# Performance work log

Measured on AMD Instinct MI355X. Metric: run time of the kernel, lower is better.

Reference implementation:

```python
import jax, jax.numpy as jnp
import numpy as np
import math

B, T, C, H = 4, 2048, 1024, 16
D = C // H  # head dim = 64


def setup_inputs() -> dict:
    key = jax.random.key(0)
    k1, k2, k3, k4, k5 = jax.random.split(key, 5)
    scale = 1.0 / math.sqrt(C)
    return {
        "x": jax.random.normal(k1, (B, T, C), dtype=jnp.float32),
        "w_attn": jax.random.normal(k2, (C, 3 * C), dtype=jnp.float32) * scale,
        "b_attn": jax.random.normal(k3, (3 * C,), dtype=jnp.float32) * 0.02,
        "w_proj": jax.random.normal(k4, (C, C), dtype=jnp.float32) * scale,
        "b_proj": jax.random.normal(k5, (C,), dtype=jnp.float32) * 0.02,
    }


def reference(x, w_attn, b_attn, w_proj, b_proj):
    Bx, Tx, Cx = x.shape
    qkv = x @ w_attn + b_attn                      # [B,T,3C]
    q, k, v = jnp.split(qkv, 3, axis=-1)           # each [B,T,C]
    # reshape to [B,H,T,D]
    q = q.reshape(Bx, Tx, H, D).transpose(0, 2, 1, 3)
    k = k.reshape(Bx, Tx, H, D).transpose(0, 2, 1, 3)
    v = v.reshape(Bx, Tx, H, D).transpose(0, 2, 1, 3)
    att = jnp.einsum("bhqd,bhkd->bhqk", q, k) * (1.0 / math.sqrt(D))
    causal = jnp.tril(jnp.ones((Tx, Tx), dtype=bool))
    att = jnp.where(causal, att, -jnp.inf)
    att = jax.nn.softmax(att, axis=-1)
    y = jnp.einsum("bhqk,bhkd->bhqd", att, v)      # [B,H,T,D]
    y = y.transpose(0, 2, 1, 3).reshape(Bx, Tx, Cx)
    return y @ w_proj + b_proj
```

## Files before the change

kernel.cpp:

```cpp
#include <hip/hip_runtime.h>
#include <hip/hip_bf16.h>
#include <stdint.h>

typedef unsigned short u16;
typedef unsigned int u32;
typedef __attribute__((ext_vector_type(8))) __bf16 bf16x8;
typedef __attribute__((ext_vector_type(4))) float f32x4;
typedef __attribute__((ext_vector_type(16))) float f32x16;

#define B_ 4
#define T_ 2048
#define C_ 1024
#define H_ 16
#define D_ 64

__device__ __forceinline__ u16 f2bf(float f) {
  union { float f; u32 u; } v; v.f = f;
  u32 r = (v.u + 0x7fffu + ((v.u >> 16) & 1u)) >> 16;
  return (u16)r;
}

__device__ __forceinline__ float fexp2(float x) {
  float r;
  asm("v_exp_f32 %0, %1\n\ts_nop 0" : "=v"(r) : "v"(x));
  return r;
}

__device__ __forceinline__ u32 cvtpk(float lo, float hi2) {
  u32 r;
  asm("v_cvt_pk_bf16_f32 %0, %1, %2" : "=v"(r) : "v"(lo), "v"(hi2));
  return r;
}

__device__ __forceinline__ void gll16(const void* g, void* l) {
  __builtin_amdgcn_global_load_lds((const __attribute__((address_space(1))) void*)g,
                                   (__attribute__((address_space(3))) void*)l, 16, 0, 0);
}

__global__ void k_prep(const float* __restrict__ x, u16* __restrict__ xb,
                       const float* __restrict__ wa, u16* __restrict__ waT,
                       const float* __restrict__ wp, u16* __restrict__ wpT) {
  __shared__ float tile[32][33];
  const int bid = blockIdx.x;
  const int tx = threadIdx.x, ty = threadIdx.y;
  if (bid < 2048) {
    const int tid = bid * 256 + ty * 32 + tx;
    const int n4 = (B_ * T_ * C_) / 4;
    for (int i = tid; i < n4; i += 2048 * 256) {
      float4 v = ((const float4*)x)[i];
      ushort4 o;
      o.x = f2bf(v.x); o.y = f2bf(v.y); o.z = f2bf(v.z); o.w = f2bf(v.w);
      ((ushort4*)xb)[i] = o;
    }
    return;
  }
  const float* src; u16* dst; int N, b2;
  if (bid < 5120) { b2 = bid - 2048; src = wa; dst = waT; N = 3 * C_; }
  else            { b2 = bid - 5120; src = wp; dst = wpT; N = C_; }
  const int K = C_;
  const int k0 = (b2 & 31) * 32, n0 = (b2 >> 5) * 32;
#pragma unroll
  for (int r = 0; r < 4; ++r) {
    int k = ty + r * 8;
    tile[k][tx] = src[(size_t)(k0 + k) * N + n0 + tx];
  }
  __syncthreads();
#pragma unroll
  for (int r = 0; r < 4; ++r) {
    int n = ty + r * 8;
    dst[(size_t)(n0 + n) * K + k0 + tx] = f2bf(tile[tx][n]);
  }
}

template <int MODE>
__global__ __launch_bounds__(256) void k_gemm(
    const u16* __restrict__ A, const u16* __restrict__ BT, const float* __restrict__ bias,
    float* __restrict__ outF, u16* __restrict__ qb, u16* __restrict__ kb, u16* __restrict__ vbT,
    int M, int N, int K) {
  __shared__ u16 al[3][128 * 32];
  __shared__ u16 bl[3][128 * 32];
  const int lane = threadIdx.x & 63, wid = threadIdx.x >> 6;
  const int nbx = N >> 7;
  const int cpx = ((M >> 7) * nbx) >> 3;
  const int wg = blockIdx.x;
  const int lid = (wg & 7) * cpx + (wg >> 3);
  const int brow = (lid / nbx) * 128, bcol = (lid % nbx) * 128;
  const int wr = (wid >> 1) * 64, wc = (wid & 1) * 64;
  const int lr = lane & 15, lg = lane >> 4;
  const int ck = (lg ^ ((lr >> 1) & 3)) * 8;
  f32x4 acc[4][4] = {};

  auto stage = [&](u16* ad, u16* bd, int t2) {
    const int kt = t2 * 32;
#pragma unroll
    for (int it = 0; it < 2; ++it) {
      int cbase = (wid * 2 + it) * 64;
      int c = cbase + lane;
      int row = c >> 2;
      int j = (c & 3) ^ ((row >> 1) & 3);
      int col = j * 8;
      gll16(A + (size_t)(brow + row) * K + kt + col, ad + cbase * 8);
      gll16(BT + (size_t)(bcol + row) * K + kt + col, bd + cbase * 8);
    }
  };

  const int nt = K / 32;
  stage(al[0], bl[0], 0);
  stage(al[1], bl[1], 1);

  for (int t = 0; t < nt; ++t) {
    if (t == nt - 1) { asm volatile("s_waitcnt vmcnt(0)" ::: "memory"); }
    else             { asm volatile("s_waitcnt vmcnt(4)" ::: "memory"); }
    __builtin_amdgcn_sched_barrier(0);
    __builtin_amdgcn_s_barrier();
    __builtin_amdgcn_sched_barrier(0);

    const int nxt = t + 2;
    if (nxt < nt) {
      const int ib = nxt % 3;
      stage(al[ib], bl[ib], nxt);
    }

    const u16* ab = al[t % 3];
    const u16* bb = bl[t % 3];
    bf16x8 af[4], bfr[4];
#pragma unroll
    for (int m = 0; m < 4; ++m) af[m] = *(const bf16x8*)&ab[(wr + m * 16 + lr) * 32 + ck];
#pragma unroll
    for (int n = 0; n < 4; ++n) bfr[n] = *(const bf16x8*)&bb[(wc + n * 16 + lr) * 32 + ck];

    __builtin_amdgcn_s_setprio(1);
#pragma unroll
    for (int m = 0; m < 4; ++m)
#pragma unroll
      for (int n = 0; n < 4; ++n)
        acc[m][n] = __builtin_amdgcn_mfma_f32_16x16x32_bf16(af[m], bfr[n], acc[m][n], 0, 0, 0);
    __builtin_amdgcn_s_setprio(0);
  }

#pragma unroll
  for (int m = 0; m < 4; ++m) {
    int row = brow + wr + m * 16 + lg * 4;
#pragma unroll
    for (int n = 0; n < 4; ++n) {
      int col = bcol + wc + n * 16 + lr;
      float bs = bias[col];
      if (MODE == 0) {
#pragma unroll
        for (int r = 0; r < 4; ++r)
          outF[(size_t)(row + r) * N + col] = acc[m][n][r] + bs;
      } else {
        int sec = col >> 10, cc = col & 1023;
        int h = cc >> 6, dd = cc & 63;
        int b = row >> 11, t = row & 2047;
        size_t bh = (size_t)(b * H_ + h);
        if (sec < 2) {
          u16* dst = (sec == 0 ? qb : kb) + (bh * T_ + t) * D_ + dd;
#pragma unroll
          for (int r = 0; r < 4; ++r) dst[(size_t)r * D_] = f2bf(acc[m][n][r] + bs);
        } else {
          ushort4 pk;
          pk.x = f2bf(acc[m][n][0] + bs);
          pk.y = f2bf(acc[m][n][1] + bs);
          pk.z = f2bf(acc[m][n][2] + bs);
          pk.w = f2bf(acc[m][n][3] + bs);
          *(ushort4*)&vbT[(bh * D_ + dd) * T_ + t] = pk;
        }
      }
    }
  }
}

__global__ __launch_bounds__(256) void k_attn(
    const u16* __restrict__ qb, const u16* __restrict__ kb,
    const u16* __restrict__ vbT, u16* __restrict__ attb) {
  __shared__ u16 kl0[64 * 64], kl1[64 * 64];
  __shared__ u16 vl0[64 * 64], vl1[64 * 64];
  const int lane = threadIdx.x & 63, wid = threadIdx.x >> 6;
  const int w = blockIdx.x;
  const int lid = (w & 7) * 64 + (w >> 3);
  const int bh = lid >> 3, qpair = lid & 7;
  const int b = bh >> 4, h = bh & 15;
  const int l31 = lane & 31, hi = lane >> 5;
  const int sw3 = l31 & 7;

  const float SC = 0.18033688f;

  const u16* kbase = kb + (size_t)bh * T_ * D_;
  const u16* vbase = vbT + (size_t)bh * D_ * T_;

  auto stage = [&](u16* kd, u16* vd, int kt) {
    const int k0 = kt * 64;
#pragma unroll
    for (int it = 0; it < 2; ++it) {
      int cbase = (wid * 2 + it) * 64;
      int c = cbase + lane;
      int cs = (c & ~7) | ((c ^ (c >> 3)) & 7);
      gll16(kbase + (size_t)k0 * D_ + (size_t)cs * 8, kd + cbase * 8);
      int vrow = cs >> 3, vcol = (cs & 7) * 8;
      gll16(vbase + (size_t)vrow * T_ + k0 + vcol, vd + cbase * 8);
    }
  };

  auto pack = [&](const f32x16& s, bf16x8* out) {
#pragma unroll
    for (int cc = 0; cc < 2; ++cc) {
      const int rb = cc * 8;
      u32 a  = cvtpk(s[rb + 0], s[rb + 1]);
      u32 c  = cvtpk(s[rb + 2], s[rb + 3]);
      u32 bb = cvtpk(s[rb + 4], s[rb + 5]);
      u32 d  = cvtpk(s[rb + 6], s[rb + 7]);
      u32 as = __shfl_xor(a, 32, 64), cs = __shfl_xor(c, 32, 64);
      u32 bs = __shfl_xor(bb, 32, 64), ds = __shfl_xor(d, 32, 64);
      union { u32 u[4]; bf16x8 v; } t;
      t.u[0] = hi ? bs : a;
      t.u[1] = hi ? ds : c;
      t.u[2] = hi ? bb : as;
      t.u[3] = hi ? d : cs;
      out[cc] = t.v;
    }
  };

#pragma unroll 1
  for (int pass = 0; pass < 2; ++pass) {
    const int qbk = pass ? (15 - qpair) : qpair;
    const int qw = qbk * 128 + wid * 32;

    const u16* qrow = qb + ((size_t)bh * T_ + qw + l31) * D_ + hi * 8;
    bf16x8 qf[4];
#pragma unroll
    for (int j = 0; j < 4; ++j) qf[j] = *(const bf16x8*)(qrow + j * 16);

    float lsum = 0.f;
    f32x16 o0 = {}, o1 = {};

    const int nt = 2 * qbk + 2;
    const int lastkt = (qw + 31) >> 6;

    auto compute = [&](const u16* kl, const u16* vl, int kt) {
      const int k0 = kt * 64;
      f32x16 s0 = {}, s1 = {};
      __builtin_amdgcn_s_setprio(1);
#pragma unroll
      for (int j = 0; j < 4; ++j) {
        const int ch = ((2 * j + hi) ^ sw3) << 3;
        const bf16x8 kf0 = *(const bf16x8*)&kl[l31 * 64 + ch];
        const bf16x8 kf1 = *(const bf16x8*)&kl[(l31 + 32) * 64 + ch];
        s0 = __builtin_amdgcn_mfma_f32_32x32x16_bf16(kf0, qf[j], s0, 0, 0, 0);
        s1 = __builtin_amdgcn_mfma_f32_32x32x16_bf16(kf1, qf[j], s1, 0, 0, 0);
      }
      __builtin_amdgcn_s_setprio(0);

      if (kt == lastkt) {
        const int q = qw + l31;
#pragma unroll
        for (int r = 0; r < 16; ++r) {
          const int kv = k0 + (r & 3) + 8 * (r >> 2) + 4 * hi;
          if (kv > q) s0[r] = -3e38f;
          if (kv + 32 > q) s1[r] = -3e38f;
        }
      }

#pragma unroll
      for (int r = 0; r < 16; ++r) s0[r] = fexp2(s0[r] * SC);
      float t0[8];
#pragma unroll
      for (int r = 0; r < 8; ++r) t0[r] = s0[r] + s0[r + 8];
#pragma unroll
      for (int w2 = 4; w2 >= 1; w2 >>= 1)
#pragma unroll
        for (int r = 0; r < 4; ++r)
          if (r < w2) t0[r] += t0[r + w2];

      bf16x8 pb0[2];
      pack(s0, pb0);
      __builtin_amdgcn_s_setprio(1);
#pragma unroll
      for (int c = 0; c < 2; ++c) {
        const int ch = ((2 * c + hi) ^ sw3) << 3;
        const bf16x8 vf0 = *(const bf16x8*)&vl[l31 * 64 + ch];
        const bf16x8 vf1 = *(const bf16x8*)&vl[(l31 + 32) * 64 + ch];
        o0 = __builtin_amdgcn_mfma_f32_32x32x16_bf16(vf0, pb0[c], o0, 0, 0, 0);
        o1 = __builtin_amdgcn_mfma_f32_32x32x16_bf16(vf1, pb0[c], o1, 0, 0, 0);
      }
      __builtin_amdgcn_s_setprio(0);

#pragma unroll
      for (int r = 0; r < 16; ++r) s1[r] = fexp2(s1[r] * SC);
      float t1[8];
#pragma unroll
      for (int r = 0; r < 8; ++r) t1[r] = s1[r] + s1[r + 8];
#pragma unroll
      for (int w2 = 4; w2 >= 1; w2 >>= 1)
#pragma unroll
        for (int r = 0; r < 4; ++r)
          if (r < w2) t1[r] += t1[r + w2];

      bf16x8 pb1[2];
      pack(s1, pb1);
      __builtin_amdgcn_s_setprio(1);
#pragma unroll
      for (int c = 2; c < 4; ++c) {
        const int ch = ((2 * c + hi) ^ sw3) << 3;
        const bf16x8 vf0 = *(const bf16x8*)&vl[l31 * 64 + ch];
        const bf16x8 vf1 = *(const bf16x8*)&vl[(l31 + 32) * 64 + ch];
        o0 = __builtin_amdgcn_mfma_f32_32x32x16_bf16(vf0, pb1[c - 2], o0, 0, 0, 0);
        o1 = __builtin_amdgcn_mfma_f32_32x32x16_bf16(vf1, pb1[c - 2], o1, 0, 0, 0);
      }
      __builtin_amdgcn_s_setprio(0);

      float ps = t0[0] + t1[0];
      ps += __shfl_xor(ps, 32, 64);
      lsum += ps;
    };

    stage(kl0, vl0, 0);
    __syncthreads();
    int kt = 0;
    while (true) {
      if (kt + 1 < nt) stage(kl1, vl1, kt + 1);
      if (kt <= lastkt) compute(kl0, vl0, kt);
      __syncthreads();
      if (++kt >= nt) break;
      if (kt + 1 < nt) stage(kl0, vl0, kt + 1);
      if (kt <= lastkt) compute(kl1, vl1, kt);
      __syncthreads();
      if (++kt >= nt) break;
    }

    const float inv = 1.0f / lsum;
    u16* orow = attb + ((size_t)b * T_ + qw + l31) * C_ + h * D_;
#pragma unroll
    for (int rg = 0; rg < 4; ++rg) {
      ushort4 w0, w1;
      w0.x = f2bf(o0[rg * 4 + 0] * inv); w0.y = f2bf(o0[rg * 4 + 1] * inv);
      w0.z = f2bf(o0[rg * 4 + 2] * inv); w0.w = f2bf(o0[rg * 4 + 3] * inv);
      w1.x = f2bf(o1[rg * 4 + 0] * inv); w1.y = f2bf(o1[rg * 4 + 1] * inv);
      w1.z = f2bf(o1[rg * 4 + 2] * inv); w1.w = f2bf(o1[rg * 4 + 3] * inv);
      const int d0 = rg * 8 + hi * 4;
      *(ushort4*)(orow + d0) = w0;
      *(ushort4*)(orow + d0 + 32) = w1;
    }
  }
}

extern "C" void kernel_launch(void* const* d_in, const int* in_sizes, int n_in,
                              void* d_out, int out_size, void* d_ws, size_t ws_size,
                              hipStream_t stream) {
  const float* x = (const float*)d_in[0];
  const float* w_attn = (const float*)d_in[1];
  const float* b_attn = (const float*)d_in[2];
  const float* w_proj = (const float*)d_in[3];
  const float* b_proj = (const float*)d_in[4];
  float* out = (float*)d_out;

  char* ws = (char*)d_ws;
  const size_t MB = 1024 * 1024;
  u16* xb   = (u16*)(ws);
  u16* attb = xb;
  u16* waT  = (u16*)(ws + 16 * MB);
  u16* wpT  = (u16*)(ws + 22 * MB);
  u16* qb   = (u16*)(ws + 24 * MB);
  u16* kb   = (u16*)(ws + 40 * MB);
  u16* vbT  = (u16*)(ws + 56 * MB);

  k_prep<<<6144, dim3(32, 8), 0, stream>>>(x, xb, w_attn, waT, w_proj, wpT);

  k_gemm<1><<<(8192 / 128) * (3 * C_ / 128), 256, 0, stream>>>(
      xb, waT, b_attn, nullptr, qb, kb, vbT, B_ * T_, 3 * C_, C_);

  k_attn<<<512, 256, 0, stream>>>(qb, kb, vbT, attb);

  k_gemm<0><<<(8192 / 128) * (C_ / 128), 256, 0, stream>>>(
      attb, wpT, b_proj, out, nullptr, nullptr, nullptr, B_ * T_, C_, C_);
}
```

Baseline: 167.5 us.

## Use 256x128 block tile GEMM for the QKV projection

Adds a new GEMM kernel with a 256x128 output tile per workgroup, where each wave computes 128x64 (8x4 MFMA tiles). It keeps a triple-buffered LDS pipeline with swizzled direct global-to-LDS loads, and uses it for the QKV projection. The larger tile raises arithmetic intensity per staged K-slice and halves the number of workgroups. In exchange it uses more accumulator registers and LDS per block, which may lower occupancy.

```diff
diff --git a/kernel.cpp b/kernel.cpp
--- a/kernel.cpp
+++ b/kernel.cpp
@@ -69,6 +69,110 @@
   for (int r = 0; r < 4; ++r) {
     int n = ty + r * 8;
     dst[(size_t)(n0 + n) * K + k0 + tx] = f2bf(tile[tx][n]);
+  }
+}
+
+template <int MODE>
+__global__ __launch_bounds__(256, 2) void k_gemmw(
+    const u16* __restrict__ A, const u16* __restrict__ BT, const float* __restrict__ bias,
+    float* __restrict__ outF, u16* __restrict__ qb, u16* __restrict__ kb, u16* __restrict__ vbT,
+    int M, int N, int K) {
+  __shared__ u16 al[3][256 * 32];
+  __shared__ u16 bl[3][128 * 32];
+  const int tid = threadIdx.x;
+  const int lane = tid & 63, wid = tid >> 6;
+  const int wm = wid >> 1, wn = wid & 1;
+  const int nbx = N >> 7;
+  const int cpx = ((M >> 8) * nbx) >> 3;
+  const int wg = blockIdx.x;
+  const int lid = (wg & 7) * cpx + (wg >> 3);
+  const int brow = (lid / nbx) * 256, bcol = (lid % nbx) * 128;
+  const int lr = lane & 15, lg = lane >> 4;
+  const int ck = (lg ^ ((lr >> 1) & 3)) * 8;
+  f32x4 acc[8][4] = {};
+
+  auto stage = [&](u16* ad, u16* bd, int t2) {
+    const int kt = t2 * 32;
+#pragma unroll
+    for (int it = 0; it < 4; ++it) {
+      int s = it * 256 + tid;
+      int row = s >> 2;
+      int j = (s & 3) ^ ((row >> 1) & 3);
+      gll16(A + (size_t)(brow + row) * K + kt + j * 8, ad + (s & ~63) * 8);
+    }
+#pragma unroll
+    for (int it = 0; it < 2; ++it) {
+      int s = it * 256 + tid;
+      int row = s >> 2;
+      int j = (s & 3) ^ ((row >> 1) & 3);
+      gll16(BT + (size_t)(bcol + row) * K + kt + j * 8, bd + (s & ~63) * 8);
+    }
+  };
+
+  const int nt = K / 32;
+  stage(al[0], bl[0], 0);
+  stage(al[1], bl[1], 1);
+
+  for (int t = 0; t < nt; ++t) {
+    if (t == nt - 1) { asm volatile("s_waitcnt vmcnt(0)" ::: "memory"); }
+    else             { asm volatile("s_waitcnt vmcnt(6)" ::: "memory"); }
+    __builtin_amdgcn_sched_barrier(0);
+    __builtin_amdgcn_s_barrier();
+    __builtin_amdgcn_sched_barrier(0);
+
+    const int nxt = t + 2;
+    if (nxt < nt) {
+      const int ib = nxt % 3;
+      stage(al[ib], bl[ib], nxt);
+    }
+
+    const u16* ab = al[t % 3];
+    const u16* bb = bl[t % 3];
+    bf16x8 af[8], bfr[4];
+#pragma unroll
+    for (int m = 0; m < 8; ++m) af[m] = *(const bf16x8*)&ab[(wm * 128 + m * 16 + lr) * 32 + ck];
+#pragma unroll
+    for (int n = 0; n < 4; ++n) bfr[n] = *(const bf16x8*)&bb[(wn * 64 + n * 16 + lr) * 32 + ck];
+
+    __builtin_amdgcn_s_setprio(1);
+#pragma unroll
+    for (int m = 0; m < 8; ++m)
+#pragma unroll
+      for (int n = 0; n < 4; ++n)
+        acc[m][n] = __builtin_amdgcn_mfma_f32_16x16x32_bf16(af[m], bfr[n], acc[m][n], 0, 0, 0);
+    __builtin_amdgcn_s_setprio(0);
+  }
+
+#pragma unroll
+  for (int m = 0; m < 8; ++m) {
+    int row = brow + wm * 128 + m * 16 + lg * 4;
+#pragma unroll
+    for (int n = 0; n < 4; ++n) {
+      int col = bcol + wn * 64 + n * 16 + lr;
+      float bs = bias[col];
+      if (MODE == 0) {
+#pragma unroll
+        for (int r = 0; r < 4; ++r)
+          outF[(size_t)(row + r) * N + col] = acc[m][n][r] + bs;
+      } else {
+        int sec = col >> 10, cc = col & 1023;
+        int h = cc >> 6, dd = cc & 63;
+        int b = row >> 11, t = row & 2047;
+        size_t bh = (size_t)(b * H_ + h);
+        if (sec < 2) {
+          u16* dst = (sec == 0 ? qb : kb) + (bh * T_ + t) * D_ + dd;
+#pragma unroll
+          for (int r = 0; r < 4; ++r) dst[(size_t)r * D_] = f2bf(acc[m][n][r] + bs);
+        } else {
+          ushort4 pk;
+          pk.x = f2bf(acc[m][n][0] + bs);
+          pk.y = f2bf(acc[m][n][1] + bs);
+          pk.z = f2bf(acc[m][n][2] + bs);
+          pk.w = f2bf(acc[m][n][3] + bs);
+          *(ushort4*)&vbT[(bh * D_ + dd) * T_ + t] = pk;
+        }
+      }
+    }
   }
 }
 
@@ -366,7 +470,7 @@
 
   k_prep<<<6144, dim3(32, 8), 0, stream>>>(x, xb, w_attn, waT, w_proj, wpT);
 
-  k_gemm<1><<<(8192 / 128) * (3 * C_ / 128), 256, 0, stream>>>(
+  k_gemmw<1><<<(8192 / 256) * (3 * C_ / 128), 256, 0, stream>>>(
       xb, waT, b_attn, nullptr, qb, kb, vbT, B_ * T_, 3 * C_, C_);
 
   k_attn<<<512, 256, 0, stream>>>(qb, kb, vbT, attb);
```

Result: slower. 180.7 us (+7.9%).

## Load K/V fragments directly from global memory instead of LDS double-buffering

Applied to the files above, without the earlier changes.

Removes the shared-memory double-buffered staging of K and V tiles and the block-wide barriers. Each wave now reads its MFMA operand fragments straight from global memory and stops at its own last causal tile instead of the block's. This drops LDS traffic and __syncthreads, but each of the four waves re-fetches the same K/V data through the cache, and the loads are no longer prefetched asynchronously ahead of compute. Global-load latency now sits directly in the MFMA dependency chain.

```diff
diff --git a/kernel.cpp b/kernel.cpp
--- a/kernel.cpp
+++ b/kernel.cpp
@@ -174,33 +174,21 @@
 __global__ __launch_bounds__(256) void k_attn(
     const u16* __restrict__ qb, const u16* __restrict__ kb,
     const u16* __restrict__ vbT, u16* __restrict__ attb) {
-  __shared__ u16 kl0[64 * 64], kl1[64 * 64];
-  __shared__ u16 vl0[64 * 64], vl1[64 * 64];
   const int lane = threadIdx.x & 63, wid = threadIdx.x >> 6;
   const int w = blockIdx.x;
   const int lid = (w & 7) * 64 + (w >> 3);
   const int bh = lid >> 3, qpair = lid & 7;
   const int b = bh >> 4, h = bh & 15;
   const int l31 = lane & 31, hi = lane >> 5;
-  const int sw3 = l31 & 7;
 
   const float SC = 0.18033688f;
 
   const u16* kbase = kb + (size_t)bh * T_ * D_;
   const u16* vbase = vbT + (size_t)bh * D_ * T_;
-
-  auto stage = [&](u16* kd, u16* vd, int kt) {
-    const int k0 = kt * 64;
-#pragma unroll
-    for (int it = 0; it < 2; ++it) {
-      int cbase = (wid * 2 + it) * 64;
-      int c = cbase + lane;
-      int cs = (c & ~7) | ((c ^ (c >> 3)) & 7);
-      gll16(kbase + (size_t)k0 * D_ + (size_t)cs * 8, kd + cbase * 8);
-      int vrow = cs >> 3, vcol = (cs & 7) * 8;
-      gll16(vbase + (size_t)vrow * T_ + k0 + vcol, vd + cbase * 8);
-    }
-  };
+  const u16* kr0 = kbase + (size_t)l31 * D_ + hi * 8;
+  const u16* kr1 = kbase + (size_t)(l31 + 32) * D_ + hi * 8;
+  const u16* vr0 = vbase + (size_t)l31 * T_ + hi * 8;
+  const u16* vr1 = vbase + (size_t)(l31 + 32) * T_ + hi * 8;
 
   auto pack = [&](const f32x16& s, bf16x8* out) {
 #pragma unroll
@@ -234,18 +222,19 @@
     float lsum = 0.f;
     f32x16 o0 = {}, o1 = {};
 
-    const int nt = 2 * qbk + 2;
     const int lastkt = (qw + 31) >> 6;
 
-    auto compute = [&](const u16* kl, const u16* vl, int kt) {
+#pragma unroll 1
+    for (int kt = 0; kt <= lastkt; ++kt) {
       const int k0 = kt * 64;
       f32x16 s0 = {}, s1 = {};
+      const u16* ka = kr0 + (size_t)k0 * D_;
+      const u16* kb2 = kr1 + (size_t)k0 * D_;
       __builtin_amdgcn_s_setprio(1);
 #pragma unroll
       for (int j = 0; j < 4; ++j) {
-        const int ch = ((2 * j + hi) ^ sw3) << 3;
-        const bf16x8 kf0 = *(const bf16x8*)&kl[l31 * 64 + ch];
-        const bf16x8 kf1 = *(const bf16x8*)&kl[(l31 + 32) * 64 + ch];
+        const bf16x8 kf0 = *(const bf16x8*)(ka + j * 16);
+        const bf16x8 kf1 = *(const bf16x8*)(kb2 + j * 16);
         s0 = __builtin_amdgcn_mfma_f32_32x32x16_bf16(kf0, qf[j], s0, 0, 0, 0);
         s1 = __builtin_amdgcn_mfma_f32_32x32x16_bf16(kf1, qf[j], s1, 0, 0, 0);
       }
@@ -261,6 +250,9 @@
         }
       }
 
+      const u16* va = vr0 + k0;
+      const u16* vb2 = vr1 + k0;
+
 #pragma unroll
       for (int r = 0; r < 16; ++r) s0[r] = fexp2(s0[r] * SC);
       float t0[8];
@@ -277,9 +269,8 @@
       __builtin_amdgcn_s_setprio(1);
 #pragma unroll
       for (int c = 0; c < 2; ++c) {
-        const int ch = ((2 * c + hi) ^ sw3) << 3;
-        const bf16x8 vf0 = *(const bf16x8*)&vl[l31 * 64 + ch];
-        const bf16x8 vf1 = *(const bf16x8*)&vl[(l31 + 32) * 64 + ch];
+        const bf16x8 vf0 = *(const bf16x8*)(va + c * 16);
+        const bf16x8 vf1 = *(const bf16x8*)(vb2 + c * 16);
         o0 = __builtin_amdgcn_mfma_f32_32x32x16_bf16(vf0, pb0[c], o0, 0, 0, 0);
         o1 = __builtin_amdgcn_mfma_f32_32x32x16_bf16(vf1, pb0[c], o1, 0, 0, 0);
       }
@@ -301,9 +292,8 @@
       __builtin_amdgcn_s_setprio(1);
 #pragma unroll
       for (int c = 2; c < 4; ++c) {
-        const int ch = ((2 * c + hi) ^ sw3) << 3;
-        const bf16x8 vf0 = *(const bf16x8*)&vl[l31 * 64 + ch];
-        const bf16x8 vf1 = *(const bf16x8*)&vl[(l31 + 32) * 64 + ch];
+        const bf16x8 vf0 = *(const bf16x8*)(va + c * 16);
+        const bf16x8 vf1 = *(const bf16x8*)(vb2 + c * 16);
         o0 = __builtin_amdgcn_mfma_f32_32x32x16_bf16(vf0, pb1[c - 2], o0, 0, 0, 0);
         o1 = __builtin_amdgcn_mfma_f32_32x32x16_bf16(vf1, pb1[c - 2], o1, 0, 0, 0);
       }
@@ -312,20 +302,6 @@
       float ps = t0[0] + t1[0];
       ps += __shfl_xor(ps, 32, 64);
       lsum += ps;
-    };
-
-    stage(kl0, vl0, 0);
-    __syncthreads();
-    int kt = 0;
-    while (true) {
-      if (kt + 1 < nt) stage(kl1, vl1, kt + 1);
-      if (kt <= lastkt) compute(kl0, vl0, kt);
-      __syncthreads();
-      if (++kt >= nt) break;
-      if (kt + 1 < nt) stage(kl0, vl0, kt + 1);
-      if (kt <= lastkt) compute(kl1, vl1, kt);
-      __syncthreads();
-      if (++kt >= nt) break;
     }
 
     const float inv = 1.0f / lsum;
```

New measurement: 233.8 us. 1.4x slower.
